# Optimization experiments

Measured on AMD Instinct MI355X. Metric: run time of the kernel, lower is better.

## Reference

```python
import jax, jax.numpy as jnp
import numpy as np

D_MODEL = 1024
N_HEADS = 16
D_K = D_MODEL // N_HEADS
B, T = 2, 2048


def setup_inputs() -> dict:
    key = jax.random.key(0)
    ks = jax.random.split(key, 12)
    s = 0.02
    return {
        "q": jax.random.normal(ks[0], (B, T, D_MODEL), jnp.float32),
        "k": jax.random.normal(ks[1], (B, T, D_MODEL), jnp.float32),
        "v": jax.random.normal(ks[2], (B, T, D_MODEL), jnp.float32),
        "Wq": jax.random.normal(ks[3], (D_MODEL, D_MODEL), jnp.float32) * s,
        "bq": jnp.zeros((D_MODEL,), jnp.float32),
        "Wk": jax.random.normal(ks[4], (D_MODEL, D_MODEL), jnp.float32) * s,
        "bk": jnp.zeros((D_MODEL,), jnp.float32),
        "Wv": jax.random.normal(ks[5], (D_MODEL, D_MODEL), jnp.float32) * s,
        "bv": jnp.zeros((D_MODEL,), jnp.float32),
        "Wo": jax.random.normal(ks[6], (D_MODEL, D_MODEL), jnp.float32) * s,
        "bo": jnp.zeros((D_MODEL,), jnp.float32),
        "mask": jnp.ones((B, T), jnp.int32),
        "causal": 1,
    }


def reference(q, k, v, Wq, bq, Wk, bk, Wv, bv, Wo, bo, mask, causal):
    Bq, Tq, D = q.shape
    Tk = k.shape[1]
    # projections (torch Linear: x @ W.T + b), split heads -> [B, H, T, d_k]
    qh = (q @ Wq.T + bq).reshape(Bq, Tq, N_HEADS, D_K).transpose(0, 2, 1, 3)
    kh = (k @ Wk.T + bk).reshape(Bq, Tk, N_HEADS, D_K).transpose(0, 2, 1, 3)
    vh = (v @ Wv.T + bv).reshape(Bq, Tk, N_HEADS, D_K).transpose(0, 2, 1, 3)
    scores = jnp.einsum("bhqd,bhkd->bhqk", qh, kh) / jnp.sqrt(jnp.float32(D_K))
    neg_inf = jnp.float32(-jnp.inf)
    if mask is not None:
        scores = jnp.where(mask[:, None, None, :] == 0, neg_inf, scores)
    if causal:
        causal_mask = jnp.tril(jnp.ones((Tq, Tq), jnp.float32))
        scores = jnp.where(causal_mask == 0, neg_inf, scores)
    attn = jax.nn.softmax(scores, axis=-1)
    out = jnp.einsum("bhqk,bhkd->bhqd", attn, vh)
    out = out.transpose(0, 2, 1, 3).reshape(Bq, Tq, D)
    return out @ Wo.T + bo
```

## Files before the change

### kernel.cpp

```cpp
#include <hip/hip_runtime.h>
#include <cstdint>
#include <cstddef>


typedef __bf16 bf16x8 __attribute__((ext_vector_type(8)));
typedef __bf16 bf16x4 __attribute__((ext_vector_type(4)));
typedef float f32x4 __attribute__((ext_vector_type(4)));

#define MFMA(a, b, c) __builtin_amdgcn_mfma_f32_16x16x32_bf16((a), (b), (c), 0, 0, 0)

static constexpr int D_MODEL = 1024;
static constexpr int T_ = 2048;
static constexpr int M_TOK = 4096;

__device__ __forceinline__ unsigned short f32_to_bf16(float f) {
    union { float f; uint32_t u; } v; v.f = f;
    uint32_t u = v.u;
    uint32_t r = u + 0x7fffu + ((u >> 16) & 1u);
    return (unsigned short)(r >> 16);
}
__device__ __forceinline__ unsigned f32_to_bf16_fast(float f) {
    union { float f; uint32_t u; } v; v.f = f;
    return (v.u + 0x8000u) >> 16;
}

typedef __attribute__((address_space(1))) void* as1_ptr;
typedef __attribute__((address_space(3))) void* as3_ptr;
__device__ __forceinline__ void gload_lds16(const void* g, void* l) {
    __builtin_amdgcn_global_load_lds((as1_ptr)(void*)g, (as3_ptr)l, 16, 0, 0);
}

__global__ __launch_bounds__(256) void cvt_all(
    const float* __restrict__ q, const float* __restrict__ k,
    const float* __restrict__ v, const float* __restrict__ wq,
    const float* __restrict__ wk, const float* __restrict__ wv,
    const float* __restrict__ wo, ushort4* __restrict__ dst) {
    int i = blockIdx.x * blockDim.x + threadIdx.x;
    constexpr int R = 1 << 20;
    const float* s;
    int idx;
    if (i < 3 * R) {
        s = (i < R) ? q : (i < 2 * R) ? k : v;
        idx = i & (R - 1);
    } else {
        int j = i - 3 * R;
        int w = j >> 18;
        s = (w == 0) ? wq : (w == 1) ? wk : (w == 2) ? wv : wo;
        idx = j & ((1 << 18) - 1);
    }
    float4 f = ((const float4*)s)[idx];
    ushort4 o;
    o.x = (unsigned short)f32_to_bf16(f.x); o.y = (unsigned short)f32_to_bf16(f.y);
    o.z = (unsigned short)f32_to_bf16(f.z); o.w = (unsigned short)f32_to_bf16(f.w);
    dst[i] = o;
}

template<int MODE>
__device__ __forceinline__ void gemm_body(
    const unsigned short* __restrict__ A, const unsigned short* __restrict__ W,
    const float* __restrict__ bias, void* __restrict__ outp,
    unsigned short* As, unsigned short* Ws, int bx, int by)
{
    constexpr bool SWAP = (MODE != 2);
    const int tid = threadIdx.x;
    const int lane = tid & 63, wave = tid >> 6;
    const int wm = wave >> 1, wn = wave & 1;
    const int r16 = lane & 15, kg = lane >> 4;
    const int m_blk = by * 128, n_blk = bx * 64;

    f32x4 acc[4][2];
    #pragma unroll
    for (int mt = 0; mt < 4; ++mt)
        #pragma unroll
        for (int nt = 0; nt < 2; ++nt) acc[mt][nt] = (f32x4){0, 0, 0, 0};

    for (int k0 = 0; k0 < D_MODEL; k0 += 64) {
        __syncthreads();
        #pragma unroll
        for (int j = 0; j < 4; ++j) {
            int si = j * 256 + tid;
            int row = si >> 3, cg = (si & 7) ^ (row & 7);
            gload_lds16(A + (size_t)(m_blk + row) * D_MODEL + k0 + cg * 8,
                        (char*)As + (j * 256 + wave * 64) * 16);
        }
        #pragma unroll
        for (int j = 0; j < 2; ++j) {
            int si = j * 256 + tid;
            int row = si >> 3, cg = (si & 7) ^ (row & 7);
            gload_lds16(W + (size_t)(n_blk + row) * D_MODEL + k0 + cg * 8,
                        (char*)Ws + (j * 256 + wave * 64) * 16);
        }
        __syncthreads();
        #pragma unroll
        for (int kc = 0; kc < 2; ++kc) {
            bf16x8 af[4], wf[2];
            #pragma unroll
            for (int mt = 0; mt < 4; ++mt) {
                int row = wm * 64 + mt * 16 + r16;
                af[mt] = *(const bf16x8*)(As + row * 64 + (((kc * 4 + kg) ^ (row & 7)) * 8));
            }
            #pragma unroll
            for (int nt = 0; nt < 2; ++nt) {
                int row = wn * 32 + nt * 16 + r16;
                wf[nt] = *(const bf16x8*)(Ws + row * 64 + (((kc * 4 + kg) ^ (row & 7)) * 8));
            }
            #pragma unroll
            for (int mt = 0; mt < 4; ++mt)
                #pragma unroll
                for (int nt = 0; nt < 2; ++nt)
                    acc[mt][nt] = SWAP ? MFMA(wf[nt], af[mt], acc[mt][nt])
                                       : MFMA(af[mt], wf[nt], acc[mt][nt]);
        }
    }
    if (MODE == 2) {
        #pragma unroll
        for (int nt = 0; nt < 2; ++nt) {
            int n = n_blk + wn * 32 + nt * 16 + r16;
            float bn = bias[n];
            int hh = n >> 6, dki = n & 63;
            #pragma unroll
            for (int mt = 0; mt < 4; ++mt) {
                int m0 = m_blk + wm * 64 + mt * 16 + kg * 4;
                int bb = m0 >> 11, ti = m0 & 2047;
                ushort4 pk;
                pk.x = f32_to_bf16(acc[mt][nt][0] + bn);
                pk.y = f32_to_bf16(acc[mt][nt][1] + bn);
                pk.z = f32_to_bf16(acc[mt][nt][2] + bn);
                pk.w = f32_to_bf16(acc[mt][nt][3] + bn);
                *(ushort4*)((unsigned short*)outp +
                    ((size_t)(bb * 16 + hh) * 64 + dki) * 2048 + ti) = pk;
            }
        }
    } else {
        #pragma unroll
        for (int nt = 0; nt < 2; ++nt) {
            int n0 = n_blk + wn * 32 + nt * 16 + kg * 4;
            float4 bn4 = *(const float4*)(bias + n0);
            #pragma unroll
            for (int mt = 0; mt < 4; ++mt) {
                int m = m_blk + wm * 64 + mt * 16 + r16;
                if (MODE == 3) {
                    float4 st;
                    st.x = acc[mt][nt][0] + bn4.x; st.y = acc[mt][nt][1] + bn4.y;
                    st.z = acc[mt][nt][2] + bn4.z; st.w = acc[mt][nt][3] + bn4.w;
                    *(float4*)((float*)outp + (size_t)m * D_MODEL + n0) = st;
                } else {
                    ushort4 pk;
                    pk.x = f32_to_bf16(acc[mt][nt][0] + bn4.x);
                    pk.y = f32_to_bf16(acc[mt][nt][1] + bn4.y);
                    pk.z = f32_to_bf16(acc[mt][nt][2] + bn4.z);
                    pk.w = f32_to_bf16(acc[mt][nt][3] + bn4.w);
                    *(ushort4*)((unsigned short*)outp + (size_t)m * D_MODEL + n0) = pk;
                }
            }
        }
    }
}

__global__ __launch_bounds__(256) void gemm_qkv(
    const unsigned short* __restrict__ qb, const unsigned short* __restrict__ kb,
    const unsigned short* __restrict__ vb, const unsigned short* __restrict__ Wqb,
    const unsigned short* __restrict__ Wkb, const unsigned short* __restrict__ Wvb,
    const float* __restrict__ bq, const float* __restrict__ bk, const float* __restrict__ bv,
    unsigned short* __restrict__ Qhp, unsigned short* __restrict__ Khp,
    unsigned short* __restrict__ Vtp)
{
    __shared__ __align__(16) unsigned short As[128 * 64];
    __shared__ __align__(16) unsigned short Ws[64 * 64];
    const int z = blockIdx.z;
    const unsigned short* A = (z == 0) ? qb : (z == 1) ? kb : vb;
    const unsigned short* W = (z == 0) ? Wqb : (z == 1) ? Wkb : Wvb;
    const float* bias = (z == 0) ? bq : (z == 1) ? bk : bv;
    if (z < 2)
        gemm_body<0>(A, W, bias, (z == 0) ? (void*)Qhp : (void*)Khp, As, Ws,
                     blockIdx.x, blockIdx.y);
    else
        gemm_body<2>(A, W, bias, (void*)Vtp, As, Ws, blockIdx.x, blockIdx.y);
}

__global__ __launch_bounds__(256) void gemm_out(
    const unsigned short* __restrict__ ab, const unsigned short* __restrict__ Wob,
    const float* __restrict__ bo, float* __restrict__ outp)
{
    __shared__ __align__(16) unsigned short As[128 * 64];
    __shared__ __align__(16) unsigned short Ws[64 * 64];
    gemm_body<3>(ab, Wob, bo, (void*)outp, As, Ws, blockIdx.x, blockIdx.y);
}

__global__ __launch_bounds__(256) void attn_fwd(
    const unsigned short* __restrict__ Qh, const unsigned short* __restrict__ Kh,
    const unsigned short* __restrict__ Vt, const int* __restrict__ mask,
    const int* __restrict__ causal_p, unsigned short* __restrict__ attnout)
{
    __shared__ __align__(16) unsigned short Ks[2][64 * 64];
    __shared__ __align__(16) unsigned short Vs[2][64 * 64];

    const int tid = threadIdx.x;
    const int lane = tid & 63, wave = tid >> 6;
    const int bh = blockIdx.x;
    const int y = blockIdx.y, y0 = y & 7, j4 = y >> 3;
    const int qc = (j4 == 0) ? y0 : (j4 == 1) ? (15 - y0)
                 : (j4 == 2) ? (16 + y0) : (31 - y0);
    const int b = bh >> 4, h = bh & 15;
    const int causal = *causal_p;
    const int r16 = lane & 15, kg = lane >> 4;

    const int q0 = qc * 64 + wave * 16;

    const unsigned short* Qb = Qh + (size_t)b * T_ * D_MODEL + h * 64;
    const unsigned short* Kb = Kh + (size_t)b * T_ * D_MODEL + h * 64;
    const unsigned short* Vb = Vt + (size_t)bh * 64 * T_;
    const int* mb = mask + b * T_;

    bf16x8 qf0 = *(const bf16x8*)(Qb + (size_t)(q0 + r16) * D_MODEL + kg * 8);
    bf16x8 qf1 = *(const bf16x8*)(Qb + (size_t)(q0 + r16) * D_MODEL + 32 + kg * 8);

    float l = 0.f;
    f32x4 o[4];
    #pragma unroll
    for (int f = 0; f < 4; ++f) o[f] = (f32x4){0, 0, 0, 0};
    const float sc2 = 0.18033688011112042f;
    const int lim = wave * 16 + r16;

    const int nT = causal ? (qc + 1) : 32;

    auto stage = [&](int buf, int t) {
        int t0 = t * 64;
        #pragma unroll
        for (int j = 0; j < 2; ++j) {
            int si = j * 256 + tid;
            int row = si >> 3, cg = (si & 7) ^ (row & 7);
            gload_lds16(Kb + (size_t)(t0 + row) * D_MODEL + cg * 8,
                        (char*)Ks[buf] + (j * 256 + wave * 64) * 16);
            gload_lds16(Vb + (size_t)row * T_ + t0 + cg * 8,
                        (char*)Vs[buf] + (j * 256 + wave * 64) * 16);
        }
    };

    stage(0, 0);
    for (int t = 0; t < nT; ++t) {
        __syncthreads();
        if (t + 1 < nT) stage((t + 1) & 1, t + 1);
        const unsigned short* Kst = Ks[t & 1];
        const unsigned short* Vst = Vs[t & 1];
        const int t0 = t * 64;
        const bool needc = causal && (t == qc);

        unsigned long long km = __ballot(mb[t0 + lane] != 0);

        f32x4 s[4];
        #pragma unroll
        for (int c = 0; c < 4; ++c) {
            int key = c * 16 + r16;
            bf16x8 kf0 = *(const bf16x8*)(Kst + key * 64 + ((kg ^ (key & 7)) * 8));
            bf16x8 kf1 = *(const bf16x8*)(Kst + key * 64 + (((4 + kg) ^ (key & 7)) * 8));
            f32x4 z = (f32x4){0, 0, 0, 0};
            z = MFMA(kf0, qf0, z);
            z = MFMA(kf1, qf1, z);
            s[c] = z;
        }

        union pk_t { unsigned u[4]; bf16x8 v; };
        pk_t pa[2];
        #pragma unroll
        for (int c = 0; c < 4; ++c) {
            unsigned mc = (unsigned)(km >> (c * 16));
            float pv[4];
            #pragma unroll
            for (int r = 0; r < 4; ++r) {
                int kbit = kg * 4 + r;
                bool mk = (mc >> kbit) & 1;
                int kk = c * 16 + kbit;
                bool ok = mk && (!needc || (kk <= lim));
                float e = ok ? __builtin_amdgcn_exp2f(s[c][r] * sc2) : 0.f;
                pv[r] = e; l += e;
            }
            int half = (c & 1) * 2;
            pa[c >> 1].u[half]     = f32_to_bf16_fast(pv[0]) | (f32_to_bf16_fast(pv[1]) << 16);
            pa[c >> 1].u[half + 1] = f32_to_bf16_fast(pv[2]) | (f32_to_bf16_fast(pv[3]) << 16);
        }

        #pragma unroll
        for (int f = 0; f < 4; ++f) {
            int row = f * 16 + r16;
            int rx = row & 7;
            #pragma unroll
            for (int cp = 0; cp < 2; ++cp) {
                int g0 = (cp * 2) * 2 + (kg >> 1);
                int g1 = (cp * 2 + 1) * 2 + (kg >> 1);
                union { bf16x4 h[2]; bf16x8 v; } vf;
                vf.h[0] = *(const bf16x4*)(Vst + row * 64 + ((g0 ^ rx) * 8) + (kg & 1) * 4);
                vf.h[1] = *(const bf16x4*)(Vst + row * 64 + ((g1 ^ rx) * 8) + (kg & 1) * 4);
                o[f] = MFMA(pa[cp].v, vf.v, o[f]);
            }
        }
    }

    l += __shfl_xor(l, 16, 64); l += __shfl_xor(l, 32, 64);
    float inv = (l > 0.f) ? 1.0f / l : 0.f;
    #pragma unroll
    for (int r = 0; r < 4; ++r) {
        int ql = kg * 4 + r;
        float iv = __shfl(inv, ql, 64);
        size_t base = ((size_t)(b * T_ + q0 + ql)) * D_MODEL + h * 64;
        #pragma unroll
        for (int f = 0; f < 4; ++f)
            attnout[base + f * 16 + r16] = f32_to_bf16(o[f][r] * iv);
    }
}

extern "C" void kernel_launch(void* const* d_in, const int* in_sizes, int n_in,
                              void* d_out, int out_size, void* d_ws, size_t ws_size,
                              hipStream_t stream) {
    const float* q  = (const float*)d_in[0];
    const float* k  = (const float*)d_in[1];
    const float* v  = (const float*)d_in[2];
    const float* Wq = (const float*)d_in[3];
    const float* bq = (const float*)d_in[4];
    const float* Wk = (const float*)d_in[5];
    const float* bk = (const float*)d_in[6];
    const float* Wv = (const float*)d_in[7];
    const float* bv = (const float*)d_in[8];
    const float* Wo = (const float*)d_in[9];
    const float* bo = (const float*)d_in[10];
    const int* mask   = (const int*)d_in[11];
    const int* causal = (const int*)d_in[12];

    const size_t SZ_TOK = (size_t)M_TOK * D_MODEL;
    const size_t SZ_W   = (size_t)D_MODEL * D_MODEL;

    unsigned short* qb  = (unsigned short*)d_ws;
    unsigned short* kb  = qb  + SZ_TOK;
    unsigned short* vb  = kb  + SZ_TOK;
    unsigned short* Wqb = vb  + SZ_TOK;
    unsigned short* Wkb = Wqb + SZ_W;
    unsigned short* Wvb = Wkb + SZ_W;
    unsigned short* Wob = Wvb + SZ_W;
    unsigned short* Qhp = Wob + SZ_W;
    unsigned short* Khp = Qhp + SZ_TOK;
    unsigned short* Vtp = Khp + SZ_TOK;
    unsigned short* ab  = Vtp + SZ_TOK;

    cvt_all<<<16384, 256, 0, stream>>>(q, k, v, Wq, Wk, Wv, Wo, (ushort4*)qb);

    gemm_qkv<<<dim3(D_MODEL / 64, M_TOK / 128, 3), 256, 0, stream>>>(
        qb, kb, vb, Wqb, Wkb, Wvb, bq, bk, bv, Qhp, Khp, Vtp);

    attn_fwd<<<dim3(32, 32), 256, 0, stream>>>(Qhp, Khp, Vtp, mask, causal, ab);

    gemm_out<<<dim3(D_MODEL / 64, M_TOK / 128), 256, 0, stream>>>(ab, Wob, bo,
                                                                  (float*)d_out);
}
```

Baseline: 233.0 us.

## Widen QKV GEMM tile, permute V keys for single bf16x8 loads, add unmasked fast path

The QKV projection GEMM now uses 128x128 tiles (NT16=4), halving the grid and re-reading each A tile fewer times, at the cost of more accumulators and LDS per block. The transposed V output is written with a key permutation so the attention PV step can fetch one contiguous bf16x8 per MFMA operand instead of two bf16x4 loads. Attention also gains a fast path that skips per-element mask and causal checks when the tile is fully unmasked and off the diagonal.

```diff
diff --git a/kernel.cpp b/kernel.cpp
--- a/kernel.cpp
+++ b/kernel.cpp
@@ -4,7 +4,6 @@
 
 
 typedef __bf16 bf16x8 __attribute__((ext_vector_type(8)));
-typedef __bf16 bf16x4 __attribute__((ext_vector_type(4)));
 typedef float f32x4 __attribute__((ext_vector_type(4)));
 
 #define MFMA(a, b, c) __builtin_amdgcn_mfma_f32_16x16x32_bf16((a), (b), (c), 0, 0, 0)
@@ -28,6 +27,10 @@
 typedef __attribute__((address_space(3))) void* as3_ptr;
 __device__ __forceinline__ void gload_lds16(const void* g, void* l) {
     __builtin_amdgcn_global_load_lds((as1_ptr)(void*)g, (as3_ptr)l, 16, 0, 0);
+}
+
+__device__ __forceinline__ int keyperm(int k) {
+    return (k & 32) | ((k & 12) << 1) | ((k & 16) >> 2) | (k & 3);
 }
 
 __global__ __launch_bounds__(256) void cvt_all(
@@ -55,7 +58,7 @@
     dst[i] = o;
 }
 
-template<int MODE>
+template<int MODE, int NT16>
 __device__ __forceinline__ void gemm_body(
     const unsigned short* __restrict__ A, const unsigned short* __restrict__ W,
     const float* __restrict__ bias, void* __restrict__ outp,
@@ -66,13 +69,13 @@
     const int lane = tid & 63, wave = tid >> 6;
     const int wm = wave >> 1, wn = wave & 1;
     const int r16 = lane & 15, kg = lane >> 4;
-    const int m_blk = by * 128, n_blk = bx * 64;
-
-    f32x4 acc[4][2];
+    const int m_blk = by * 128, n_blk = bx * (NT16 * 32);
+
+    f32x4 acc[4][NT16];
     #pragma unroll
     for (int mt = 0; mt < 4; ++mt)
         #pragma unroll
-        for (int nt = 0; nt < 2; ++nt) acc[mt][nt] = (f32x4){0, 0, 0, 0};
+        for (int nt = 0; nt < NT16; ++nt) acc[mt][nt] = (f32x4){0, 0, 0, 0};
 
     for (int k0 = 0; k0 < D_MODEL; k0 += 64) {
         __syncthreads();
@@ -84,7 +87,7 @@
                         (char*)As + (j * 256 + wave * 64) * 16);
         }
         #pragma unroll
-        for (int j = 0; j < 2; ++j) {
+        for (int j = 0; j < NT16; ++j) {
             int si = j * 256 + tid;
             int row = si >> 3, cg = (si & 7) ^ (row & 7);
             gload_lds16(W + (size_t)(n_blk + row) * D_MODEL + k0 + cg * 8,
@@ -93,35 +96,36 @@
         __syncthreads();
         #pragma unroll
         for (int kc = 0; kc < 2; ++kc) {
-            bf16x8 af[4], wf[2];
+            bf16x8 af[4], wf[NT16];
             #pragma unroll
             for (int mt = 0; mt < 4; ++mt) {
                 int row = wm * 64 + mt * 16 + r16;
                 af[mt] = *(const bf16x8*)(As + row * 64 + (((kc * 4 + kg) ^ (row & 7)) * 8));
             }
             #pragma unroll
-            for (int nt = 0; nt < 2; ++nt) {
-                int row = wn * 32 + nt * 16 + r16;
+            for (int nt = 0; nt < NT16; ++nt) {
+                int row = wn * (NT16 * 16) + nt * 16 + r16;
                 wf[nt] = *(const bf16x8*)(Ws + row * 64 + (((kc * 4 + kg) ^ (row & 7)) * 8));
             }
             #pragma unroll
             for (int mt = 0; mt < 4; ++mt)
                 #pragma unroll
-                for (int nt = 0; nt < 2; ++nt)
+                for (int nt = 0; nt < NT16; ++nt)
                     acc[mt][nt] = SWAP ? MFMA(wf[nt], af[mt], acc[mt][nt])
                                        : MFMA(af[mt], wf[nt], acc[mt][nt]);
         }
     }
     if (MODE == 2) {
         #pragma unroll
-        for (int nt = 0; nt < 2; ++nt) {
-            int n = n_blk + wn * 32 + nt * 16 + r16;
+        for (int nt = 0; nt < NT16; ++nt) {
+            int n = n_blk + wn * (NT16 * 16) + nt * 16 + r16;
             float bn = bias[n];
             int hh = n >> 6, dki = n & 63;
             #pragma unroll
             for (int mt = 0; mt < 4; ++mt) {
                 int m0 = m_blk + wm * 64 + mt * 16 + kg * 4;
-                int bb = m0 >> 11, ti = m0 & 2047;
+                int mp = (m0 & ~63) | keyperm(m0 & 63);
+                int bb = mp >> 11, ti = mp & 2047;
                 ushort4 pk;
                 pk.x = f32_to_bf16(acc[mt][nt][0] + bn);
                 pk.y = f32_to_bf16(acc[mt][nt][1] + bn);
@@ -133,8 +137,8 @@
         }
     } else {
         #pragma unroll
-        for (int nt = 0; nt < 2; ++nt) {
-            int n0 = n_blk + wn * 32 + nt * 16 + kg * 4;
+        for (int nt = 0; nt < NT16; ++nt) {
+            int n0 = n_blk + wn * (NT16 * 16) + nt * 16 + kg * 4;
             float4 bn4 = *(const float4*)(bias + n0);
             #pragma unroll
             for (int mt = 0; mt < 4; ++mt) {
@@ -166,16 +170,16 @@
     unsigned short* __restrict__ Vtp)
 {
     __shared__ __align__(16) unsigned short As[128 * 64];
-    __shared__ __align__(16) unsigned short Ws[64 * 64];
+    __shared__ __align__(16) unsigned short Ws[128 * 64];
     const int z = blockIdx.z;
     const unsigned short* A = (z == 0) ? qb : (z == 1) ? kb : vb;
     const unsigned short* W = (z == 0) ? Wqb : (z == 1) ? Wkb : Wvb;
     const float* bias = (z == 0) ? bq : (z == 1) ? bk : bv;
     if (z < 2)
-        gemm_body<0>(A, W, bias, (z == 0) ? (void*)Qhp : (void*)Khp, As, Ws,
-                     blockIdx.x, blockIdx.y);
+        gemm_body<0, 4>(A, W, bias, (z == 0) ? (void*)Qhp : (void*)Khp, As, Ws,
+                        blockIdx.x, blockIdx.y);
     else
-        gemm_body<2>(A, W, bias, (void*)Vtp, As, Ws, blockIdx.x, blockIdx.y);
+        gemm_body<2, 4>(A, W, bias, (void*)Vtp, As, Ws, blockIdx.x, blockIdx.y);
 }
 
 __global__ __launch_bounds__(256) void gemm_out(
@@ -184,7 +188,7 @@
 {
     __shared__ __align__(16) unsigned short As[128 * 64];
     __shared__ __align__(16) unsigned short Ws[64 * 64];
-    gemm_body<3>(ab, Wob, bo, (void*)outp, As, Ws, blockIdx.x, blockIdx.y);
+    gemm_body<3, 2>(ab, Wob, bo, (void*)outp, As, Ws, blockIdx.x, blockIdx.y);
 }
 
 __global__ __launch_bounds__(256) void attn_fwd(
@@ -244,7 +248,7 @@
         const unsigned short* Kst = Ks[t & 1];
         const unsigned short* Vst = Vs[t & 1];
         const int t0 = t * 64;
-        const bool needc = causal && (t == qc);
+        const bool diag = causal && (t == qc);
 
         unsigned long long km = __ballot(mb[t0 + lane] != 0);
 
@@ -260,24 +264,36 @@
             s[c] = z;
         }
 
+        float pv[4][4];
+        if (!diag && km == ~0ull) {
+            #pragma unroll
+            for (int c = 0; c < 4; ++c)
+                #pragma unroll
+                for (int r = 0; r < 4; ++r) {
+                    float e = __builtin_amdgcn_exp2f(s[c][r] * sc2);
+                    pv[c][r] = e; l += e;
+                }
+        } else {
+            #pragma unroll
+            for (int c = 0; c < 4; ++c) {
+                unsigned mc = (unsigned)(km >> (c * 16));
+                #pragma unroll
+                for (int r = 0; r < 4; ++r) {
+                    int kbit = kg * 4 + r;
+                    bool ok = ((mc >> kbit) & 1) && (!diag || (c * 16 + kbit <= lim));
+                    float e = ok ? __builtin_amdgcn_exp2f(s[c][r] * sc2) : 0.f;
+                    pv[c][r] = e; l += e;
+                }
+            }
+        }
+
         union pk_t { unsigned u[4]; bf16x8 v; };
         pk_t pa[2];
         #pragma unroll
         for (int c = 0; c < 4; ++c) {
-            unsigned mc = (unsigned)(km >> (c * 16));
-            float pv[4];
-            #pragma unroll
-            for (int r = 0; r < 4; ++r) {
-                int kbit = kg * 4 + r;
-                bool mk = (mc >> kbit) & 1;
-                int kk = c * 16 + kbit;
-                bool ok = mk && (!needc || (kk <= lim));
-                float e = ok ? __builtin_amdgcn_exp2f(s[c][r] * sc2) : 0.f;
-                pv[r] = e; l += e;
-            }
             int half = (c & 1) * 2;
-            pa[c >> 1].u[half]     = f32_to_bf16_fast(pv[0]) | (f32_to_bf16_fast(pv[1]) << 16);
-            pa[c >> 1].u[half + 1] = f32_to_bf16_fast(pv[2]) | (f32_to_bf16_fast(pv[3]) << 16);
+            pa[c >> 1].u[half]     = f32_to_bf16_fast(pv[c][0]) | (f32_to_bf16_fast(pv[c][1]) << 16);
+            pa[c >> 1].u[half + 1] = f32_to_bf16_fast(pv[c][2]) | (f32_to_bf16_fast(pv[c][3]) << 16);
         }
 
         #pragma unroll
@@ -286,12 +302,9 @@
             int rx = row & 7;
             #pragma unroll
             for (int cp = 0; cp < 2; ++cp) {
-                int g0 = (cp * 2) * 2 + (kg >> 1);
-                int g1 = (cp * 2 + 1) * 2 + (kg >> 1);
-                union { bf16x4 h[2]; bf16x8 v; } vf;
-                vf.h[0] = *(const bf16x4*)(Vst + row * 64 + ((g0 ^ rx) * 8) + (kg & 1) * 4);
-                vf.h[1] = *(const bf16x4*)(Vst + row * 64 + ((g1 ^ rx) * 8) + (kg & 1) * 4);
-                o[f] = MFMA(pa[cp].v, vf.v, o[f]);
+                int g = cp * 4 + kg;
+                bf16x8 vf = *(const bf16x8*)(Vst + row * 64 + ((g ^ rx) * 8));
+                o[f] = MFMA(pa[cp].v, vf, o[f]);
             }
         }
     }
@@ -343,7 +356,7 @@
 
     cvt_all<<<16384, 256, 0, stream>>>(q, k, v, Wq, Wk, Wv, Wo, (ushort4*)qb);
 
-    gemm_qkv<<<dim3(D_MODEL / 64, M_TOK / 128, 3), 256, 0, stream>>>(
+    gemm_qkv<<<dim3(D_MODEL / 128, M_TOK / 128, 3), 256, 0, stream>>>(
         qb, kb, vb, Wqb, Wkb, Wvb, bq, bk, bv, Qhp, Khp, Vtp);
 
     attn_fwd<<<dim3(32, 32), 256, 0, stream>>>(Qhp, Khp, Vtp, mask, causal, ab);
```

Result: faster. 225.1 us (-3.4%).
